# Performance work log

Hardware: AMD Instinct MI355X
Metric: run time of the kernel (lower is better)

## Reference

```python
import jax, jax.numpy as jnp
import numpy as np

N_NODES = 50000
N_EDGES = 600000
IN_CH = 128
OUT_CH = 128
HEADS = 1


def setup_inputs() -> dict:
    key = jax.random.key(0)
    ks = jax.random.split(key, 6)
    x = jax.random.normal(ks[0], (N_NODES, IN_CH), dtype=jnp.float32)
    edge_index = jax.random.randint(ks[1], (2, N_EDGES), 0, N_NODES, dtype=jnp.int64)
    weight = jax.random.normal(ks[2], (IN_CH, HEADS * OUT_CH), dtype=jnp.float32) * (1.0 / np.sqrt(IN_CH))
    u = jax.random.normal(ks[3], (IN_CH, HEADS), dtype=jnp.float32) * (1.0 / np.sqrt(IN_CH))
    c = jax.random.normal(ks[4], (HEADS,), dtype=jnp.float32)
    bias = jax.random.normal(ks[5], (OUT_CH,), dtype=jnp.float32) * 0.01
    return {"x": x, "edge_index": edge_index, "weight": weight, "u": u, "c": c, "bias": bias}


def reference(x, edge_index, weight, u, c, bias):
    N = x.shape[0]
    # FeaStConv default add_self_loops=True
    loops = jnp.arange(N, dtype=edge_index.dtype)
    src = jnp.concatenate([edge_index[0], loops])  # x_j (source / neighbor)
    dst = jnp.concatenate([edge_index[1], loops])  # x_i (target / center)
    # per-edge soft assignment over heads: q = softmax((x_j - x_i) @ u + c)
    q = jax.nn.softmax((x[src] - x[dst]) @ u + c, axis=1)          # [E, H]
    xj = (x[src] @ weight).reshape(-1, HEADS, OUT_CH)              # [E, H, F]
    msg = (xj * q[:, :, None]).sum(axis=1)                         # [E, F]
    # mean aggregation over incoming edges at each target node
    agg = jax.ops.segment_sum(msg, dst, num_segments=N)
    cnt = jax.ops.segment_sum(jnp.ones((dst.shape[0],), x.dtype), dst, num_segments=N)
    out = agg / jnp.maximum(cnt, 1.0)[:, None] + bias
    return jax.nn.relu(out)
```

## Files before the change

### kernel.cpp

```cpp
#include <hip/hip_runtime.h>

#define N_NODES 50000
#define N_EDGES 600000
#define CH 128
#define ROWS 32
#define AGG_BLOCKS 1563
#define MD 32
#define SPILL_CAP 65536
#define HSTRIDE 136
#define RSTRIDE 64
#define NBINS 49
#define BIN_CAP 16384
#define BIN_BLOCKS 586
#define PREP_BLOCKS 1563
#define POISON 0xAAAAAAAAu

typedef __attribute__((ext_vector_type(8))) short bf16x8;
typedef __attribute__((ext_vector_type(4))) float f32x4;
typedef __attribute__((ext_vector_type(2))) float f32x2;
typedef __attribute__((ext_vector_type(4))) unsigned short u16x4;

__device__ inline unsigned int f2bf(float f) {
    unsigned int b = __float_as_uint(f);
    unsigned int r = b + 0x7fffu + ((b >> 16) & 1u);
    return r >> 16;
}

__device__ inline f32x2 bf2(unsigned int u) {
    return (f32x2){__uint_as_float(u << 16), __uint_as_float(u & 0xffff0000u)};
}

__device__ inline void acc8(f32x2* a, int4 u) {
    a[0] += bf2((unsigned int)u.x);
    a[1] += bf2((unsigned int)u.y);
    a[2] += bf2((unsigned int)u.z);
    a[3] += bf2((unsigned int)u.w);
}

__global__ __launch_bounds__(1024) void k_bin_prep(
    const float* __restrict__ x, const float* __restrict__ Wm,
    const int* __restrict__ ei, unsigned short* __restrict__ xh,
    unsigned short* __restrict__ Wt, unsigned int* __restrict__ bincur,
    unsigned int* __restrict__ binbuf) {
    const int b = blockIdx.x;
    const int t = threadIdx.x;
    if (b < BIN_BLOCKS) {
        __shared__ unsigned int cnt[64];
        __shared__ unsigned int pfx[64];
        __shared__ unsigned int base[64];
        __shared__ unsigned int staged[1024];
        if (t < 64) cnt[t] = 0;
        __syncthreads();
        const int e = b * 1024 + t;
        int bin = 63;
        unsigned int packed = 63u << 26;
        if (e < N_EDGES) {
            int src = ei[e];
            int dst = ei[N_EDGES + e];
            bin = dst >> 10;
            packed = (unsigned int)src | ((unsigned int)(dst & 1023) << 16)
                   | ((unsigned int)bin << 26);
        }
        const unsigned int rank = atomicAdd(&cnt[bin], 1u);
        __syncthreads();
        if (t == 0) {
            unsigned int s = 0;
            for (int i = 0; i < 64; ++i) { pfx[i] = s; s += cnt[i]; }
        }
        __syncthreads();
        staged[pfx[bin] + rank] = packed;
        if (t < NBINS && cnt[t] > 0)
            base[t] = atomicAdd(&bincur[t], cnt[t]) - POISON;
        __syncthreads();
        const unsigned int p = staged[t];
        const int fb = (int)(p >> 26);
        if (fb < NBINS) {
            unsigned int pos = base[fb] + ((unsigned int)t - pfx[fb]);
            if (pos < BIN_CAP)
                binbuf[(size_t)fb * BIN_CAP + pos] = p;
        }
    } else {
        const int i = (b - BIN_BLOCKS) * 1024 + t;
        if (i < 1600000) {
            float4 v = ((const float4*)x)[i];
            ushort4 o;
            o.x = (unsigned short)f2bf(v.x);
            o.y = (unsigned short)f2bf(v.y);
            o.z = (unsigned short)f2bf(v.z);
            o.w = (unsigned short)f2bf(v.w);
            ((ushort4*)xh)[i] = o;
            if (i < CH * CH) {
                int n = i >> 7, k = i & 127;
                Wt[n * CH + k] = (unsigned short)f2bf(Wm[k * CH + n]);
            }
        }
    }
}

__global__ __launch_bounds__(1024) void k_place(
    const unsigned int* __restrict__ bincur, const unsigned int* __restrict__ binbuf,
    unsigned short* __restrict__ rec, unsigned int* __restrict__ spill_cnt,
    int* __restrict__ spill) {
    __shared__ unsigned int cnt[1024];
    __shared__ unsigned short ell[1024 * MD];
    const int b = blockIdx.x;
    const int t = threadIdx.x;
    cnt[t] = 0;
    __syncthreads();
    unsigned int nb = bincur[b] - POISON;
    if (nb > BIN_CAP) nb = BIN_CAP;
    for (unsigned int i = t; i < nb; i += 1024) {
        const unsigned int p = binbuf[(size_t)b * BIN_CAP + i];
        const unsigned int src  = p & 0xFFFFu;
        const unsigned int dloc = (p >> 16) & 1023u;
        const unsigned int r = atomicAdd(&cnt[dloc], 1u);
        if (r < MD) {
            ell[dloc * MD + r] = (unsigned short)src;
        } else {
            int pp = (int)(atomicAdd(spill_cnt, 1u) - POISON);
            if (pp >= 0 && pp < SPILL_CAP) {
                spill[2 * pp] = (int)src;
                spill[2 * pp + 1] = b * 1024 + (int)dloc;
            }
        }
    }
    __syncthreads();
    {
        const int n = b * 1024 + t;
        if (n < N_NODES)
            *(unsigned int*)(rec + (size_t)n * RSTRIDE) = cnt[t];
    }
    #pragma unroll
    for (int pzz = 0; pzz < 4; ++pzz) {
        const int nloc = pzz * 256 + (t >> 2);
        const int part = t & 3;
        const int n = b * 1024 + nloc;
        if (n < N_NODES) {
            const int4 v = *(const int4*)&ell[(size_t)pzz * 8192 + (size_t)t * 8];
            *(int4*)(rec + (size_t)n * RSTRIDE + 4 + part * 8) = v;
        }
    }
}

__global__ __launch_bounds__(512, 8) void k_agg_mfma(
    const unsigned short* __restrict__ xh, const unsigned short* __restrict__ rec,
    const unsigned int* __restrict__ spill_cnt, const int* __restrict__ spill,
    const unsigned short* __restrict__ Wt, const float* __restrict__ bias,
    float* __restrict__ out) {
    __shared__ __align__(16) unsigned short HsB[ROWS * HSTRIDE];
    const int t = threadIdx.x;
    const int wv = t >> 6;
    const int lane = t & 63;
    const int quad = lane >> 4;
    const int l16 = lane & 15;
    const int row0 = blockIdx.x * ROWS;
    const int c8 = l16 * 8;

    {
        const int ln = wv * 4 + quad;
        const int n = row0 + ln;
        if (n < N_NODES) {
            const unsigned short* rp = rec + (size_t)n * RSTRIDE;
            f32x2 a[4];
            a[0] = (f32x2){0.f, 0.f}; a[1] = (f32x2){0.f, 0.f};
            a[2] = (f32x2){0.f, 0.f}; a[3] = (f32x2){0.f, 0.f};
            acc8(a, *(const int4*)(xh + (size_t)n * CH + c8));
            const int d = (int)*(const unsigned int*)rp;
            const int dl = (d < MD) ? d : MD;
            const unsigned short* cl = rp + 4;
            int j = 0;
            for (; j + 3 < dl; j += 4) {
                u16x4 c = *(const u16x4*)(cl + j);
                int4 u0 = *(const int4*)(xh + (size_t)c[0] * CH + c8);
                int4 u1 = *(const int4*)(xh + (size_t)c[1] * CH + c8);
                int4 u2 = *(const int4*)(xh + (size_t)c[2] * CH + c8);
                int4 u3 = *(const int4*)(xh + (size_t)c[3] * CH + c8);
                acc8(a, u0); acc8(a, u1); acc8(a, u2); acc8(a, u3);
            }
            for (; j < dl; ++j)
                acc8(a, *(const int4*)(xh + (size_t)cl[j] * CH + c8));
            int sc = (int)(*spill_cnt - POISON);
            if (sc > 0) {
                if (sc > SPILL_CAP) sc = SPILL_CAP;
                for (int sidx = 0; sidx < sc; ++sidx) {
                    if (spill[2 * sidx + 1] == n)
                        acc8(a, *(const int4*)(xh + (size_t)spill[2 * sidx] * CH + c8));
                }
            }
            const float inv = 1.0f / (float)(d + 1);
            int4 p;
            p.x = (int)(f2bf(a[0].x * inv) | (f2bf(a[0].y * inv) << 16));
            p.y = (int)(f2bf(a[1].x * inv) | (f2bf(a[1].y * inv) << 16));
            p.z = (int)(f2bf(a[2].x * inv) | (f2bf(a[2].y * inv) << 16));
            p.w = (int)(f2bf(a[3].x * inv) | (f2bf(a[3].y * inv) << 16));
            *(int4*)&HsB[ln * HSTRIDE + c8] = p;
        }
    }

    const int ncol = wv * 16 + l16;
    bf16x8 bfr[4];
    #pragma unroll
    for (int ks = 0; ks < 4; ++ks)
        bfr[ks] = *(const bf16x8*)(Wt + (size_t)ncol * CH + ks * 32 + quad * 8);
    const float bv = bias[ncol];

    __syncthreads();

    f32x4 acc0 = (f32x4){0.f, 0.f, 0.f, 0.f};
    f32x4 acc1 = (f32x4){0.f, 0.f, 0.f, 0.f};
    #pragma unroll
    for (int ks = 0; ks < 4; ++ks) {
        bf16x8 af0 = *(const bf16x8*)(&HsB[l16 * HSTRIDE + quad * 8 + ks * 32]);
        bf16x8 af1 = *(const bf16x8*)(&HsB[(16 + l16) * HSTRIDE + quad * 8 + ks * 32]);
        acc0 = __builtin_amdgcn_mfma_f32_16x16x32_bf16(af0, bfr[ks], acc0, 0, 0, 0);
        acc1 = __builtin_amdgcn_mfma_f32_16x16x32_bf16(af1, bfr[ks], acc1, 0, 0, 0);
    }

    #pragma unroll
    for (int r = 0; r < 4; ++r) {
        const int row = row0 + quad * 4 + r;
        __builtin_nontemporal_store(fmaxf(acc0[r] + bv, 0.f),
                                    &out[(size_t)row * CH + ncol]);
    }
    #pragma unroll
    for (int r = 0; r < 4; ++r) {
        const int row = row0 + 16 + quad * 4 + r;
        if (row < N_NODES)
            __builtin_nontemporal_store(fmaxf(acc1[r] + bv, 0.f),
                                        &out[(size_t)row * CH + ncol]);
    }
}

extern "C" void kernel_launch(void* const* d_in, const int* in_sizes, int n_in,
                              void* d_out, int out_size, void* d_ws, size_t ws_size,
                              hipStream_t stream) {
    const float* x    = (const float*)d_in[0];
    const int*   ei   = (const int*)d_in[1];
    const float* Wm   = (const float*)d_in[2];
    const float* bias = (const float*)d_in[5];
    float* out = (float*)d_out;

    const size_t xh_bytes   = (size_t)N_NODES * CH * 2;
    const size_t wt_bytes   = (size_t)CH * CH * 2;
    const size_t rec_bytes  = (size_t)N_NODES * RSTRIDE * 2;
    const size_t bin_bytes  = (size_t)NBINS * BIN_CAP * 4;

    unsigned short* xh     = (unsigned short*)d_ws;
    unsigned short* Wt     = (unsigned short*)((char*)d_ws + xh_bytes);
    unsigned short* rec    = (unsigned short*)((char*)d_ws + xh_bytes + wt_bytes);
    unsigned int*   binbuf = (unsigned int*)((char*)d_ws + xh_bytes + wt_bytes + rec_bytes);
    unsigned int*   bincur = (unsigned int*)((char*)d_ws + xh_bytes + wt_bytes + rec_bytes + bin_bytes);
    unsigned int*   spill_cnt = bincur + 64;
    int*            spill  = (int*)(spill_cnt + 1);

    k_bin_prep<<<dim3(BIN_BLOCKS + PREP_BLOCKS), dim3(1024), 0, stream>>>(
        x, Wm, ei, xh, Wt, bincur, binbuf);
    k_place<<<dim3(NBINS), dim3(1024), 0, stream>>>(
        bincur, binbuf, rec, spill_cnt, spill);
    k_agg_mfma<<<dim3(AGG_BLOCKS), dim3(512), 0, stream>>>(
        xh, rec, spill_cnt, spill, Wt, bias, out);
}
```

Measured before the change: 134.8 us.

## Split bin counters into groups and quarter k_place blocks by destination range

Each destination bin's global cursor becomes eight per-group cursors, selected by block index, so fewer binning blocks contend on the same atomic. The k_place kernel now launches four blocks per bin, each handling a 256-node quarter, which raises parallelism from 49 blocks to 196 and shrinks shared memory per block. The serial prefix sum is replaced with a wavefront shuffle scan. In exchange, each k_place block reads every entry of its bin and discards three quarters of them, and per-group capacity of 2048 could overflow if the edge distribution is skewed.

```diff
diff --git a/kernel.cpp b/kernel.cpp
--- a/kernel.cpp
+++ b/kernel.cpp
@@ -10,7 +10,8 @@
 #define HSTRIDE 136
 #define RSTRIDE 64
 #define NBINS 49
-#define BIN_CAP 16384
+#define NGRP 8
+#define CAP_G 2048
 #define BIN_BLOCKS 586
 #define PREP_BLOCKS 1563
 #define POISON 0xAAAAAAAAu
@@ -63,21 +64,28 @@
         }
         const unsigned int rank = atomicAdd(&cnt[bin], 1u);
         __syncthreads();
-        if (t == 0) {
-            unsigned int s = 0;
-            for (int i = 0; i < 64; ++i) { pfx[i] = s; s += cnt[i]; }
+        if (t < 64) {
+            const unsigned int c = cnt[t];
+            unsigned int s = c;
+            #pragma unroll
+            for (int off = 1; off < 64; off <<= 1) {
+                unsigned int v = __shfl_up(s, off, 64);
+                if (t >= off) s += v;
+            }
+            pfx[t] = s - c;
         }
         __syncthreads();
         staged[pfx[bin] + rank] = packed;
+        const int g = b & (NGRP - 1);
         if (t < NBINS && cnt[t] > 0)
-            base[t] = atomicAdd(&bincur[t], cnt[t]) - POISON;
+            base[t] = atomicAdd(&bincur[t * NGRP + g], cnt[t]) - POISON;
         __syncthreads();
         const unsigned int p = staged[t];
         const int fb = (int)(p >> 26);
         if (fb < NBINS) {
             unsigned int pos = base[fb] + ((unsigned int)t - pfx[fb]);
-            if (pos < BIN_CAP)
-                binbuf[(size_t)fb * BIN_CAP + pos] = p;
+            if (pos < CAP_G)
+                binbuf[((size_t)fb * NGRP + g) * CAP_G + pos] = p;
         }
     } else {
         const int i = (b - BIN_BLOCKS) * 1024 + t;
@@ -101,42 +109,46 @@
     const unsigned int* __restrict__ bincur, const unsigned int* __restrict__ binbuf,
     unsigned short* __restrict__ rec, unsigned int* __restrict__ spill_cnt,
     int* __restrict__ spill) {
-    __shared__ unsigned int cnt[1024];
-    __shared__ unsigned short ell[1024 * MD];
-    const int b = blockIdx.x;
+    __shared__ unsigned int cnt[256];
+    __shared__ unsigned short ell[256 * MD];
+    const int bq = blockIdx.x;
+    const int b = bq >> 2;
+    const int q = bq & 3;
     const int t = threadIdx.x;
-    cnt[t] = 0;
+    if (t < 256) cnt[t] = 0;
     __syncthreads();
-    unsigned int nb = bincur[b] - POISON;
-    if (nb > BIN_CAP) nb = BIN_CAP;
-    for (unsigned int i = t; i < nb; i += 1024) {
-        const unsigned int p = binbuf[(size_t)b * BIN_CAP + i];
-        const unsigned int src  = p & 0xFFFFu;
-        const unsigned int dloc = (p >> 16) & 1023u;
-        const unsigned int r = atomicAdd(&cnt[dloc], 1u);
-        if (r < MD) {
-            ell[dloc * MD + r] = (unsigned short)src;
-        } else {
-            int pp = (int)(atomicAdd(spill_cnt, 1u) - POISON);
-            if (pp >= 0 && pp < SPILL_CAP) {
-                spill[2 * pp] = (int)src;
-                spill[2 * pp + 1] = b * 1024 + (int)dloc;
+    for (int g = 0; g < NGRP; ++g) {
+        unsigned int nb = bincur[b * NGRP + g] - POISON;
+        if (nb > CAP_G) nb = CAP_G;
+        for (unsigned int i = t; i < nb; i += 1024) {
+            const unsigned int p = binbuf[((size_t)b * NGRP + g) * CAP_G + i];
+            const unsigned int dloc = (p >> 16) & 1023u;
+            if ((int)(dloc >> 8) == q) {
+                const unsigned int r = atomicAdd(&cnt[dloc & 255u], 1u);
+                if (r < MD) {
+                    ell[(dloc & 255u) * MD + r] = (unsigned short)(p & 0xFFFFu);
+                } else {
+                    int pp = (int)(atomicAdd(spill_cnt, 1u) - POISON);
+                    if (pp >= 0 && pp < SPILL_CAP) {
+                        spill[2 * pp] = (int)(p & 0xFFFFu);
+                        spill[2 * pp + 1] = b * 1024 + (int)dloc;
+                    }
+                }
             }
         }
     }
     __syncthreads();
-    {
-        const int n = b * 1024 + t;
+    if (t < 256) {
+        const int n = b * 1024 + q * 256 + t;
         if (n < N_NODES)
             *(unsigned int*)(rec + (size_t)n * RSTRIDE) = cnt[t];
     }
-    #pragma unroll
-    for (int pzz = 0; pzz < 4; ++pzz) {
-        const int nloc = pzz * 256 + (t >> 2);
+    {
+        const int nloc = t >> 2;
         const int part = t & 3;
-        const int n = b * 1024 + nloc;
+        const int n = b * 1024 + q * 256 + nloc;
         if (n < N_NODES) {
-            const int4 v = *(const int4*)&ell[(size_t)pzz * 8192 + (size_t)t * 8];
+            const int4 v = *(const int4*)&ell[(size_t)nloc * MD + part * 8];
             *(int4*)(rec + (size_t)n * RSTRIDE + 4 + part * 8) = v;
         }
     }
@@ -243,19 +255,19 @@
     const size_t xh_bytes   = (size_t)N_NODES * CH * 2;
     const size_t wt_bytes   = (size_t)CH * CH * 2;
     const size_t rec_bytes  = (size_t)N_NODES * RSTRIDE * 2;
-    const size_t bin_bytes  = (size_t)NBINS * BIN_CAP * 4;
+    const size_t bin_bytes  = (size_t)NBINS * NGRP * CAP_G * 4;
 
     unsigned short* xh     = (unsigned short*)d_ws;
     unsigned short* Wt     = (unsigned short*)((char*)d_ws + xh_bytes);
     unsigned short* rec    = (unsigned short*)((char*)d_ws + xh_bytes + wt_bytes);
     unsigned int*   binbuf = (unsigned int*)((char*)d_ws + xh_bytes + wt_bytes + rec_bytes);
     unsigned int*   bincur = (unsigned int*)((char*)d_ws + xh_bytes + wt_bytes + rec_bytes + bin_bytes);
-    unsigned int*   spill_cnt = bincur + 64;
+    unsigned int*   spill_cnt = bincur + 512;
     int*            spill  = (int*)(spill_cnt + 1);
 
     k_bin_prep<<<dim3(BIN_BLOCKS + PREP_BLOCKS), dim3(1024), 0, stream>>>(
         x, Wm, ei, xh, Wt, bincur, binbuf);
-    k_place<<<dim3(NBINS), dim3(1024), 0, stream>>>(
+    k_place<<<dim3(NBINS * 4), dim3(1024), 0, stream>>>(
         bincur, binbuf, rec, spill_cnt, spill);
     k_agg_mfma<<<dim3(AGG_BLOCKS), dim3(512), 0, stream>>>(
         xh, rec, spill_cnt, spill, Wt, bias, out);
```

New measurement: 135.6 us. About the same (+0.6%).
